# Kernel tuning notes

Hardware: AMD Instinct MI355X
Metric: run time of the kernel (lower is better)

Reference implementation:

```python
import jax, jax.numpy as jnp
import numpy as np

MAX_DISP = 48


def setup_inputs() -> dict:
    key = jax.random.key(0)
    k1, k2 = jax.random.split(key)
    left = jax.random.normal(k1, (2, 64, 256, 32), dtype=jnp.float32)
    right = jax.random.normal(k2, (2, 64, 256, 32), dtype=jnp.float32)
    return {"left": left, "right": right}


def reference(left, right):
    # left, right: [B, H, W, C] NHWC feature maps.
    # For each disparity d in [-D, D): out[b, d+D, h, w] = concat(left[b,h,w], right[b,h,w-d])
    # where positions with (w - d) out of [0, W) are zeroed (matches TF concat+pad semantics:
    # the pad zeroes BOTH the left and right channel halves in the invalid region).
    B, H, W, C = left.shape
    disps = jnp.arange(-MAX_DISP, MAX_DISP)          # [2D]
    w_idx = jnp.arange(W)                            # [W]

    def level(d):
        idx = w_idx - d                              # right-image column for each output column
        valid = (idx >= 0) & (idx < W)               # [W]
        r = jnp.take(right, jnp.clip(idx, 0, W - 1), axis=2)   # [B,H,W,C]
        lvl = jnp.concatenate([left, r], axis=-1)               # [B,H,W,2C]
        return jnp.where(valid[None, None, :, None], lvl, jnp.zeros((), lvl.dtype))

    cv = jax.vmap(level)(disps)                      # [2D, B, H, W, 2C]
    return jnp.transpose(cv, (1, 0, 2, 3, 4))        # [B, 2D, H, W, 2C]
```

## Files before the change

kernel.cpp:

```cpp
#include <hip/hip_runtime.h>


typedef float f4 __attribute__((ext_vector_type(4)));

#define DD_STRIDE 262144

__global__ __launch_bounds__(256) void cost_concat_kernel(
    const f4* __restrict__ left4,
    const f4* __restrict__ right4,
    f4* __restrict__ out4)
{
    const int tid = blockIdx.x * 256 + threadIdx.x;
    const int c3 = tid & 7;
    const int w  = (tid >> 3) & 255;
    const int s  = (tid >> 11) & 1;
    const int hb = tid >> 12;
    const int b  = hb >> 6;
    const int h  = hb & 63;

    const int rowBase = hb * 2048;

    f4* optr = out4 + (size_t)b * 25165824 + (size_t)h * 4096
                    + (size_t)(w * 16 + s * 8 + c3);

    const int dd_lo = max(0, w - 207);
    const int dd_hi = min(95, w + 48);
    const f4 z = (f4){0.f, 0.f, 0.f, 0.f};

    int dd = 0;
    for (; dd < dd_lo; ++dd)
        __builtin_nontemporal_store(z, optr + (size_t)dd * DD_STRIDE);

    if (s == 0) {
        const f4 v = left4[rowBase + w * 8 + c3];
        #pragma unroll 4
        for (; dd <= dd_hi; ++dd)
            __builtin_nontemporal_store(v, optr + (size_t)dd * DD_STRIDE);
    } else {
        const f4* rp = right4 + rowBase + (w + 48) * 8 + c3;
        #pragma unroll 4
        for (; dd <= dd_hi; ++dd)
            __builtin_nontemporal_store(rp[-(ptrdiff_t)dd * 8], optr + (size_t)dd * DD_STRIDE);
    }

    for (; dd < 96; ++dd)
        __builtin_nontemporal_store(z, optr + (size_t)dd * DD_STRIDE);
}

extern "C" void kernel_launch(void* const* d_in, const int* in_sizes, int n_in,
                              void* d_out, int out_size, void* d_ws, size_t ws_size,
                              hipStream_t stream) {
    const f4* left4  = (const f4*)d_in[0];
    const f4* right4 = (const f4*)d_in[1];
    f4* out4 = (f4*)d_out;

    cost_concat_kernel<<<2048, 256, 0, stream>>>(left4, right4, out4);
}
```

Measured before the change: 178.0 us.

## Stage row inputs in LDS and emit contiguous output rows per disparity block

Each block now loads a full left and right row (b,h) into shared memory and writes 24 disparity levels, each as a contiguous 4 KB-per-row store across threads. The earlier version had each thread stride across disparities and reload from global memory. The grid shrinks from 2048 to 512 blocks. Stores become regular (non-nontemporal) and fully coalesced per disparity level, but 64 KB of LDS per block limits occupancy and the nontemporal hint is dropped.

```diff
diff --git a/kernel.cpp b/kernel.cpp
--- a/kernel.cpp
+++ b/kernel.cpp
@@ -10,41 +10,47 @@
     const f4* __restrict__ right4,
     f4* __restrict__ out4)
 {
-    const int tid = blockIdx.x * 256 + threadIdx.x;
-    const int c3 = tid & 7;
-    const int w  = (tid >> 3) & 255;
-    const int s  = (tid >> 11) & 1;
-    const int hb = tid >> 12;
-    const int b  = hb >> 6;
-    const int h  = hb & 63;
+    __shared__ f4 lds[4096];
 
+    const int t   = threadIdx.x;
+    const int blk = blockIdx.x;
+    const int g   = blk & 3;
+    const int hb  = blk >> 2;
     const int rowBase = hb * 2048;
 
-    f4* optr = out4 + (size_t)b * 25165824 + (size_t)h * 4096
-                    + (size_t)(w * 16 + s * 8 + c3);
+    #pragma unroll
+    for (int k = 0; k < 8; ++k)
+        lds[k * 256 + t] = left4[rowBase + k * 256 + t];
+    #pragma unroll
+    for (int k = 0; k < 8; ++k)
+        lds[2048 + k * 256 + t] = right4[rowBase + k * 256 + t];
+    __syncthreads();
 
-    const int dd_lo = max(0, w - 207);
-    const int dd_hi = min(95, w + 48);
-    const f4 z = (f4){0.f, 0.f, 0.f, 0.f};
+    const int c4  = t & 15;
+    const int wb  = t >> 4;
+    const bool isLeft = c4 < 8;
+    const int cc  = c4 & 7;
+    const int b   = hb >> 6;
+    const int h   = hb & 63;
+    const int dd0 = g * 24;
 
-    int dd = 0;
-    for (; dd < dd_lo; ++dd)
-        __builtin_nontemporal_store(z, optr + (size_t)dd * DD_STRIDE);
+    f4* orow = out4 + (size_t)b * 25165824 + (size_t)dd0 * DD_STRIDE + (size_t)h * 4096;
 
-    if (s == 0) {
-        const f4 v = left4[rowBase + w * 8 + c3];
-        #pragma unroll 4
-        for (; dd <= dd_hi; ++dd)
-            __builtin_nontemporal_store(v, optr + (size_t)dd * DD_STRIDE);
-    } else {
-        const f4* rp = right4 + rowBase + (w + 48) * 8 + c3;
-        #pragma unroll 4
-        for (; dd <= dd_hi; ++dd)
-            __builtin_nontemporal_store(rp[-(ptrdiff_t)dd * 8], optr + (size_t)dd * DD_STRIDE);
+    for (int k = 0; k < 24; ++k) {
+        const int d = dd0 + k - 48;
+        f4* op = orow + (size_t)k * DD_STRIDE + t;
+        #pragma unroll
+        for (int j = 0; j < 16; ++j) {
+            const int w   = j * 16 + wb;
+            const int idx = w - d;
+            const bool valid = (unsigned)idx < 256u;
+            const int ci  = valid ? idx : 0;
+            const int la  = isLeft ? (w * 8 + cc) : (2048 + ci * 8 + cc);
+            f4 v = lds[la];
+            v = valid ? v : (f4){0.f, 0.f, 0.f, 0.f};
+            op[j * 256] = v;
+        }
     }
-
-    for (; dd < 96; ++dd)
-        __builtin_nontemporal_store(z, optr + (size_t)dd * DD_STRIDE);
 }
 
 extern "C" void kernel_launch(void* const* d_in, const int* in_sizes, int n_in,
@@ -54,5 +60,5 @@
     const f4* right4 = (const f4*)d_in[1];
     f4* out4 = (f4*)d_out;
 
-    cost_concat_kernel<<<2048, 256, 0, stream>>>(left4, right4, out4);
+    cost_concat_kernel<<<512, 256, 0, stream>>>(left4, right4, out4);
 }
```

Result: faster. 148.9 us (median of 2 runs) (-16.3%).
